# Optimization experiments

Hardware: AMD Instinct MI355X
Metric: run time of the kernel (lower is better)

Reference implementation:

```python
import jax, jax.numpy as jnp
import numpy as np

B, S, H, M, E = 8, 2048, 2048, 256, 8
Hh = H // 2

def setup_inputs() -> dict:
    key = jax.random.key(0)
    ks = jax.random.split(key, 12)
    s = 0.02
    return {
        "x":   jax.random.normal(ks[0], (B, S, H), dtype=jnp.float32),
        # metacognitive (router) network: H -> M -> M -> E, softmax
        "Wm1": jax.random.normal(ks[1], (H, M), dtype=jnp.float32) * s,
        "bm1": jnp.zeros((M,), dtype=jnp.float32),
        "Wm2": jax.random.normal(ks[2], (M, M), dtype=jnp.float32) * s,
        "bm2": jnp.zeros((M,), dtype=jnp.float32),
        "Wm3": jax.random.normal(ks[3], (M, E), dtype=jnp.float32) * s,
        "bm3": jnp.zeros((E,), dtype=jnp.float32),
        # stacked expert MLPs: Linear(H,H/2)-ReLU-Linear(H/2,H)-Tanh
        "W1":  jax.random.normal(ks[4], (E, H, Hh), dtype=jnp.float32) * s,
        "b1":  jnp.zeros((E, Hh), dtype=jnp.float32),
        "W2":  jax.random.normal(ks[5], (E, Hh, H), dtype=jnp.float32) * s,
        "b2":  jnp.zeros((E, H), dtype=jnp.float32),
        # strategy_effectiveness buffer (init: ones)
        "eff": jnp.ones((E,), dtype=jnp.float32),
    }

def reference(x, Wm1, bm1, Wm2, bm2, Wm3, bm3, W1, b1, W2, b2, eff):
    # --- select_strategy ---
    pooled = x.mean(axis=1)                                   # [B,H]
    h = jax.nn.relu(pooled @ Wm1 + bm1)                       # [B,M]
    h = jax.nn.relu(h @ Wm2 + bm2)                            # [B,M]
    probs = jax.nn.softmax(h @ Wm3 + bm3, axis=-1)            # [B,E]
    w = jax.nn.softmax(probs * eff[None, :], axis=-1)         # [B,E]
    # --- apply_strategies (all experts batched) ---
    he = jax.nn.relu(jnp.einsum('bsh,ehf->bsef', x, W1) + b1) # [B,S,E,Hh]
    ye = jnp.tanh(jnp.einsum('bsef,efh->bseh', he, W2) + b2)  # [B,S,E,H]
    out = jnp.einsum('bseh,be->bsh', ye, w)                   # [B,S,H]
    return out
```

## Files before the change

kernel.cpp:

```cpp
#include <hip/hip_runtime.h>
#include <hip/hip_bf16.h>
#include <cstdint>
#include <cstddef>

#define B_   8
#define S_   2048
#define H_   2048
#define M_   256
#define E_   8
#define HH_  1024
#define BS_  (B_*S_)

typedef _Float16 f16;
typedef _Float16 f16x8 __attribute__((ext_vector_type(8)));
typedef _Float16 f16x4 __attribute__((ext_vector_type(4)));
typedef float    f32x4 __attribute__((ext_vector_type(4)));

#define HSLOT 32768

__device__ __forceinline__ void gl_lds16(const void* g, void* l) {
  __builtin_amdgcn_global_load_lds(
      (const __attribute__((address_space(1))) uint32_t*)g,
      (__attribute__((address_space(3))) uint32_t*)l, 16, 0, 0);
}

__device__ __forceinline__ float fast_tanh(float x) {
  x = fminf(fmaxf(x, -15.f), 15.f);
  float t = __expf(2.f * x);
  return (t - 1.f) / (t + 1.f);
}

template<int NG, bool SEG, int KB, class F>
__device__ __forceinline__ void kloop(const char* aBlk, const char* bBlk,
                                      char* ldsc, f32x4 (&acc)[8][4], F&& fold) {
  constexpr int NH = NG * 2;
  const int tid = threadIdx.x, ln = tid & 63, wv = tid >> 6;
  const int l15 = ln & 15, kq = ln >> 4;
  const int wm = wv >> 2, wn = wv & 3;

  const char* aPc[2]; const char* bPc[2];
#pragma unroll
  for (int j = 0; j < 2; ++j) {
    int row = (tid >> 2) + j * 128;
    int kqs = (tid & 3) ^ ((row >> 1) & 3);
    aPc[j] = aBlk + (size_t)row * KB + kqs * 16;
    bPc[j] = bBlk + (size_t)row * KB + kqs * 16;
  }
  const int rowA = wm * 128 + l15;
  const int rowB = wn * 64 + l15;
  const int aRd = rowA * 64 + ((kq ^ ((rowA >> 1) & 3)) << 4);
  const int bRd = 16384 + rowB * 64 + ((kq ^ ((rowB >> 1) & 3)) << 4);
  const int dst0 = tid * 16;

  auto stage2 = [&](int Ht, int op) {
    if (Ht >= NH) return;
    char* sb = ldsc + (Ht & 3) * HSLOT;
    size_t oa, ob;
    if constexpr (SEG) {
      size_t kb = (size_t)((Ht & 31) * 64);
      oa = ((size_t)(Ht >> 5) << 25) + kb;
      ob = ((size_t)(Ht >> 5) << 22) + kb;
    } else { oa = ob = (size_t)Ht * 64; }
    if (op == 0) {
      gl_lds16(aPc[0] + oa, sb + dst0);
      gl_lds16(aPc[1] + oa, sb + 8192 + dst0);
    } else {
      gl_lds16(bPc[0] + ob, sb + 16384 + dst0);
      gl_lds16(bPc[1] + ob, sb + 24576 + dst0);
    }
  };

#pragma unroll
  for (int Ht = 0; Ht < 3; ++Ht) { stage2(Ht, 0); stage2(Ht, 1); }
  asm volatile("s_waitcnt vmcnt(8)" ::: "memory");
  __builtin_amdgcn_s_barrier();

#pragma unroll 1
  for (int g = 0; g < NG; ++g) {
#pragma unroll
    for (int kh = 0; kh < 2; ++kh) {
      const int H = g * 2 + kh;
      const char* sb = ldsc + (H & 3) * HSLOT;
      f16x8 bf[4];
#pragma unroll
      for (int mh = 0; mh < 2; ++mh) {
        f16x8 af[4];
        const char* ab = sb + aRd + mh * 4096;
#pragma unroll
        for (int m = 0; m < 4; ++m) af[m] = *(const f16x8*)(ab + m * 1024);
        if (mh == 0) {
          const char* bb = sb + bRd;
#pragma unroll
          for (int n = 0; n < 4; ++n) bf[n] = *(const f16x8*)(bb + n * 1024);
        }
        stage2(H + 3, mh);
        __builtin_amdgcn_s_barrier();
        __builtin_amdgcn_s_setprio(1);
#pragma unroll
        for (int m = 0; m < 4; ++m)
#pragma unroll
          for (int n = 0; n < 4; ++n)
            acc[mh * 4 + m][n] = __builtin_amdgcn_mfma_f32_16x16x32_f16(
                af[m], bf[n], acc[mh * 4 + m][n], 0, 0, 0);
        __builtin_amdgcn_s_setprio(0);
        if (mh == 1) {
          if (H < NH - 3)       { asm volatile("s_waitcnt vmcnt(8)" ::: "memory"); }
          else if (H == NH - 3) { asm volatile("s_waitcnt vmcnt(4)" ::: "memory"); }
          else if (H == NH - 2) { asm volatile("s_waitcnt vmcnt(0)" ::: "memory"); }
        }
        __builtin_amdgcn_s_barrier();
      }
    }
    if constexpr (SEG) { if ((g & 15) == 15) fold(g >> 4); }
  }
}

__global__ __launch_bounds__(512, 2) void gemm1_t8(
    const f16* __restrict__ xf, const f16* __restrict__ W1t,
    const float* __restrict__ b1, f16* __restrict__ he) {
  __shared__ alignas(16) char ldsc[4 * HSLOT];
  int id = blockIdx.x;
  int logical = (id & 7) * 256 + (id >> 3);
  int e = logical >> 8, mt = (logical >> 2) & 63, nt = logical & 3;
  int brow = mt * 256, bcol = nt * 256;

  const char* aBlk = (const char*)xf + (size_t)brow * 4096;
  const char* bBlk = (const char*)W1t + ((size_t)e << 22) + (size_t)bcol * 4096;

  f32x4 acc[8][4] = {};
  kloop<32, false, 4096>(aBlk, bBlk, ldsc, acc, [](int) {});

  const int tid = threadIdx.x, ln = tid & 63, wv = tid >> 6;
  const int l15 = ln & 15, kq4 = (ln >> 4) * 4;
  const int wm = wv >> 2, wn = wv & 3;
  f16* C = he + ((size_t)e << 24);
#pragma unroll
  for (int n = 0; n < 4; ++n) {
    int gc = bcol + wn * 64 + n * 16 + l15;
    float bias = b1[e * HH_ + gc];
#pragma unroll
    for (int m = 0; m < 8; ++m) {
      int gr0 = brow + wm * 128 + m * 16 + kq4;
#pragma unroll
      for (int r = 0; r < 4; ++r)
        C[(size_t)(gr0 + r) * HH_ + gc] = (f16)fmaxf(acc[m][n][r] + bias, 0.f);
    }
  }
}

__global__ __launch_bounds__(512, 2) void gemm2_t8(
    const f16* __restrict__ he, const f16* __restrict__ W2t,
    const float* __restrict__ b2, const float* __restrict__ wbuf,
    float* __restrict__ out) {
  __shared__ alignas(16) char ldsc[4 * HSLOT];
  __shared__ float biasLDS[E_][256];
  __shared__ float wLDS[E_];
  int id = blockIdx.x;
  int logical = (id & 7) * 64 + (id >> 3);
  int mt = logical >> 3, nt = logical & 7;
  int brow = mt * 256, bcol = nt * 256;
  int bb = brow >> 11;

  const int tid = threadIdx.x, ln = tid & 63, wv = tid >> 6;
  const int l15 = ln & 15, kq4 = (ln >> 4) * 4;
  const int wm = wv >> 2, wn = wv & 3;

  {
    int i = tid;
#pragma unroll
    for (int rep = 0; rep < 4; ++rep, i += 512)
      biasLDS[i >> 8][i & 255] = b2[(size_t)(i >> 8) * H_ + bcol + (i & 255)];
    if (tid < E_) wLDS[tid] = wbuf[bb * E_ + tid];
  }
  __syncthreads();

  const char* aBlk = (const char*)he + (size_t)brow * 2048;
  const char* bBlk = (const char*)W2t + (size_t)bcol * 2048;

  f32x4 acc[8][4] = {};
  f16x4 tot[8][4] = {};

  auto fold = [&](int e) {
    float we = wLDS[e];
#pragma unroll
    for (int n = 0; n < 4; ++n) {
      float bias = biasLDS[e][wn * 64 + n * 16 + l15];
#pragma unroll
      for (int m = 0; m < 8; ++m) {
#pragma unroll
        for (int r = 0; r < 4; ++r) {
          tot[m][n][r] += (f16)(we * fast_tanh(acc[m][n][r] + bias));
          acc[m][n][r] = 0.f;
        }
      }
    }
  };

  kloop<128, true, 2048>(aBlk, bBlk, ldsc, acc, fold);

#pragma unroll
  for (int n = 0; n < 4; ++n) {
    int gc = bcol + wn * 64 + n * 16 + l15;
#pragma unroll
    for (int m = 0; m < 8; ++m) {
      int gr0 = brow + wm * 128 + m * 16 + kq4;
#pragma unroll
      for (int r = 0; r < 4; ++r)
        out[(size_t)(gr0 + r) * H_ + gc] = (float)tot[m][n][r];
    }
  }
}

__global__ void convert_x_pool(const float* __restrict__ x, f16* __restrict__ xf,
                               float* __restrict__ partial) {
  int h  = blockIdx.x * 256 + threadIdx.x;
  int sc = blockIdx.y;
  int b  = blockIdx.z;
  size_t base = ((size_t)b * S_ + sc * 64) * H_ + h;
  float sum = 0.f;
#pragma unroll 4
  for (int i = 0; i < 64; ++i) {
    float v = x[base + (size_t)i * H_];
    sum += v;
    xf[base + (size_t)i * H_] = (f16)v;
  }
  partial[((size_t)b * H_ + h) * 32 + sc] = sum;
}

__global__ void pool_finalize(const float* __restrict__ partial, float* __restrict__ pooled) {
  int i = blockIdx.x * 256 + threadIdx.x;
  float s = 0.f;
#pragma unroll
  for (int c = 0; c < 32; ++c) s += partial[(size_t)i * 32 + c];
  pooled[i] = s * (1.0f / S_);
}

__global__ void router_kernel(const float* __restrict__ pooled,
                              const float* __restrict__ Wm1, const float* __restrict__ bm1,
                              const float* __restrict__ Wm2, const float* __restrict__ bm2,
                              const float* __restrict__ Wm3, const float* __restrict__ bm3,
                              const float* __restrict__ eff, float* __restrict__ wout) {
  __shared__ float pl[H_];
  __shared__ float h1[M_];
  __shared__ float h2[M_];
  __shared__ float lg[E_];
  int b = blockIdx.x;
  int t = threadIdx.x;

  for (int i = t; i < H_; i += 256) pl[i] = pooled[b * H_ + i];
  __syncthreads();

  float s = bm1[t];
  for (int k = 0; k < H_; ++k) s += pl[k] * Wm1[(size_t)k * M_ + t];
  h1[t] = fmaxf(s, 0.f);
  __syncthreads();

  s = bm2[t];
  for (int k = 0; k < M_; ++k) s += h1[k] * Wm2[k * M_ + t];
  h2[t] = fmaxf(s, 0.f);
  __syncthreads();

  if (t < E_) {
    float l = bm3[t];
    for (int k = 0; k < M_; ++k) l += h2[k] * Wm3[k * E_ + t];
    lg[t] = l;
  }
  __syncthreads();

  if (t == 0) {
    float p[E_], q[E_];
    float mx = -1e30f;
    for (int e = 0; e < E_; ++e) mx = fmaxf(mx, lg[e]);
    float den = 0.f;
    for (int e = 0; e < E_; ++e) { p[e] = __expf(lg[e] - mx); den += p[e]; }
    float inv = 1.f / den;
    for (int e = 0; e < E_; ++e) q[e] = p[e] * inv * eff[e];
    mx = -1e30f;
    for (int e = 0; e < E_; ++e) mx = fmaxf(mx, q[e]);
    den = 0.f;
    for (int e = 0; e < E_; ++e) { q[e] = __expf(q[e] - mx); den += q[e]; }
    inv = 1.f / den;
    for (int e = 0; e < E_; ++e) wout[b * E_ + e] = q[e] * inv;
  }
}

__global__ void transpose_cvt(const float* __restrict__ in, f16* __restrict__ out,
                              int R, int C) {
  __shared__ f16 tile[32][33];
  int e  = blockIdx.z;
  int c0 = blockIdx.x * 32, r0 = blockIdx.y * 32;
  int tx = threadIdx.x & 31, ty = threadIdx.x >> 5;
  const float* inp = in + (size_t)e * R * C;
  f16* outp = out + (size_t)e * R * C;
#pragma unroll
  for (int i = 0; i < 4; ++i) {
    int r = r0 + ty + i * 8;
    tile[ty + i * 8][tx] = (f16)inp[(size_t)r * C + c0 + tx];
  }
  __syncthreads();
#pragma unroll
  for (int i = 0; i < 4; ++i) {
    int c = c0 + ty + i * 8;
    outp[(size_t)c * R + r0 + tx] = tile[tx][ty + i * 8];
  }
}

extern "C" void kernel_launch(void* const* d_in, const int* in_sizes, int n_in,
                              void* d_out, int out_size, void* d_ws, size_t ws_size,
                              hipStream_t stream) {
  const float* x   = (const float*)d_in[0];
  const float* Wm1 = (const float*)d_in[1];
  const float* bm1 = (const float*)d_in[2];
  const float* Wm2 = (const float*)d_in[3];
  const float* bm2 = (const float*)d_in[4];
  const float* Wm3 = (const float*)d_in[5];
  const float* bm3 = (const float*)d_in[6];
  const float* W1  = (const float*)d_in[7];
  const float* b1  = (const float*)d_in[8];
  const float* W2  = (const float*)d_in[9];
  const float* b2  = (const float*)d_in[10];
  const float* eff = (const float*)d_in[11];
  float* out = (float*)d_out;

  char* ws = (char*)d_ws;
  size_t off = 0;
  auto take = [&](size_t bytes) { void* p = ws + off; off += (bytes + 255) & ~(size_t)255; return p; };

  f16*   xf      = (f16*)  take((size_t)BS_ * H_ * 2);
  f16*   W1t     = (f16*)  take((size_t)E_ * HH_ * H_ * 2);
  f16*   W2t     = (f16*)  take((size_t)E_ * H_ * HH_ * 2);
  float* partial = (float*)take((size_t)B_ * H_ * 32 * 4);
  float* pooled  = (float*)take((size_t)B_ * H_ * 4);
  float* wbuf    = (float*)take(1024);
  f16*   he      = (f16*)  take((size_t)E_ * BS_ * HH_ * 2);

  convert_x_pool<<<dim3(H_ / 256, S_ / 64, B_), 256, 0, stream>>>(x, xf, partial);
  pool_finalize<<<(B_ * H_) / 256, 256, 0, stream>>>(partial, pooled);
  router_kernel<<<B_, 256, 0, stream>>>(pooled, Wm1, bm1, Wm2, bm2, Wm3, bm3, eff, wbuf);
  transpose_cvt<<<dim3(HH_ / 32, H_ / 32, E_), 256, 0, stream>>>(W1, W1t, H_, HH_);
  transpose_cvt<<<dim3(H_ / 32, HH_ / 32, E_), 256, 0, stream>>>(W2, W2t, HH_, H_);

  gemm1_t8<<<2048, 512, 0, stream>>>(xf, W1t, b1, he);
  gemm2_t8<<<512, 512, 0, stream>>>(he, W2t, b2, wbuf, out);
}
```

Baseline: 1.420 ms.

## Double-buffer LDS fragment registers to overlap LDS reads with MFMA in k-loop

Restructures the GEMM k-loop so register fragments for the next half-tile are read from LDS while MFMAs run on the current fragments, using ping-pong register sets (af0/af1, bfE/bfO). It removes one of the two barriers per half-step and retunes the vmcnt waits to the new issue order of global-to-LDS loads. This costs more live registers, which may pressure occupancy at 2 waves/SIMD with 512 threads. The reduced barrier count also makes LDS slot reuse correctness depend on the new wait placement.

```diff
diff --git a/kernel.cpp b/kernel.cpp
--- a/kernel.cpp
+++ b/kernel.cpp
@@ -70,47 +70,83 @@
     }
   };
 
-#pragma unroll
-  for (int Ht = 0; Ht < 3; ++Ht) { stage2(Ht, 0); stage2(Ht, 1); }
+  f16x8 af0[4], af1[4], bfE[4], bfO[4];
+
+#pragma unroll
+  for (int t = 0; t < 3; ++t) { stage2(t, 0); stage2(t, 1); }
   asm volatile("s_waitcnt vmcnt(8)" ::: "memory");
   __builtin_amdgcn_s_barrier();
+  {
+    const char* s0 = ldsc;
+#pragma unroll
+    for (int m = 0; m < 4; ++m) af0[m] = *(const f16x8*)(s0 + aRd + m * 1024);
+#pragma unroll
+    for (int n = 0; n < 4; ++n) bfE[n] = *(const f16x8*)(s0 + bRd + n * 1024);
+  }
 
 #pragma unroll 1
   for (int g = 0; g < NG; ++g) {
-#pragma unroll
-    for (int kh = 0; kh < 2; ++kh) {
-      const int H = g * 2 + kh;
-      const char* sb = ldsc + (H & 3) * HSLOT;
-      f16x8 bf[4];
-#pragma unroll
-      for (int mh = 0; mh < 2; ++mh) {
-        f16x8 af[4];
-        const char* ab = sb + aRd + mh * 4096;
-#pragma unroll
-        for (int m = 0; m < 4; ++m) af[m] = *(const f16x8*)(ab + m * 1024);
-        if (mh == 0) {
-          const char* bb = sb + bRd;
-#pragma unroll
-          for (int n = 0; n < 4; ++n) bf[n] = *(const f16x8*)(bb + n * 1024);
-        }
-        stage2(H + 3, mh);
-        __builtin_amdgcn_s_barrier();
-        __builtin_amdgcn_s_setprio(1);
-#pragma unroll
-        for (int m = 0; m < 4; ++m)
-#pragma unroll
-          for (int n = 0; n < 4; ++n)
-            acc[mh * 4 + m][n] = __builtin_amdgcn_mfma_f32_16x16x32_f16(
-                af[m], bf[n], acc[mh * 4 + m][n], 0, 0, 0);
-        __builtin_amdgcn_s_setprio(0);
-        if (mh == 1) {
-          if (H < NH - 3)       { asm volatile("s_waitcnt vmcnt(8)" ::: "memory"); }
-          else if (H == NH - 3) { asm volatile("s_waitcnt vmcnt(4)" ::: "memory"); }
-          else if (H == NH - 2) { asm volatile("s_waitcnt vmcnt(0)" ::: "memory"); }
-        }
-        __builtin_amdgcn_s_barrier();
-      }
-    }
+    const int H0 = 2 * g;
+    const char* s0 = ldsc + (H0 & 3) * HSLOT;
+    const char* s1 = ldsc + ((H0 + 1) & 3) * HSLOT;
+
+#pragma unroll
+    for (int m = 0; m < 4; ++m) af1[m] = *(const f16x8*)(s0 + aRd + 4096 + m * 1024);
+    stage2(H0 + 3, 0);
+    __builtin_amdgcn_s_setprio(1);
+#pragma unroll
+    for (int m = 0; m < 4; ++m)
+#pragma unroll
+      for (int n = 0; n < 4; ++n)
+        acc[m][n] = __builtin_amdgcn_mfma_f32_16x16x32_f16(af0[m], bfE[n], acc[m][n], 0, 0, 0);
+    __builtin_amdgcn_s_setprio(0);
+
+    if (g < NG - 1) { asm volatile("s_waitcnt vmcnt(6)" ::: "memory"); }
+    else            { asm volatile("s_waitcnt vmcnt(0)" ::: "memory"); }
+    __builtin_amdgcn_s_barrier();
+#pragma unroll
+    for (int m = 0; m < 4; ++m) af0[m] = *(const f16x8*)(s1 + aRd + m * 1024);
+#pragma unroll
+    for (int n = 0; n < 4; ++n) bfO[n] = *(const f16x8*)(s1 + bRd + n * 1024);
+    stage2(H0 + 3, 1);
+    __builtin_amdgcn_s_setprio(1);
+#pragma unroll
+    for (int m = 0; m < 4; ++m)
+#pragma unroll
+      for (int n = 0; n < 4; ++n)
+        acc[4 + m][n] = __builtin_amdgcn_mfma_f32_16x16x32_f16(af1[m], bfE[n], acc[4 + m][n], 0, 0, 0);
+    __builtin_amdgcn_s_setprio(0);
+
+#pragma unroll
+    for (int m = 0; m < 4; ++m) af1[m] = *(const f16x8*)(s1 + aRd + 4096 + m * 1024);
+    stage2(H0 + 4, 0);
+    __builtin_amdgcn_s_setprio(1);
+#pragma unroll
+    for (int m = 0; m < 4; ++m)
+#pragma unroll
+      for (int n = 0; n < 4; ++n)
+        acc[m][n] = __builtin_amdgcn_mfma_f32_16x16x32_f16(af0[m], bfO[n], acc[m][n], 0, 0, 0);
+    __builtin_amdgcn_s_setprio(0);
+
+    if (g < NG - 1) {
+      if (g < NG - 2) { asm volatile("s_waitcnt vmcnt(6)" ::: "memory"); }
+      else            { asm volatile("s_waitcnt vmcnt(4)" ::: "memory"); }
+      __builtin_amdgcn_s_barrier();
+      const char* s2 = ldsc + ((H0 + 2) & 3) * HSLOT;
+#pragma unroll
+      for (int m = 0; m < 4; ++m) af0[m] = *(const f16x8*)(s2 + aRd + m * 1024);
+#pragma unroll
+      for (int n = 0; n < 4; ++n) bfE[n] = *(const f16x8*)(s2 + bRd + n * 1024);
+    }
+    stage2(H0 + 4, 1);
+    __builtin_amdgcn_s_setprio(1);
+#pragma unroll
+    for (int m = 0; m < 4; ++m)
+#pragma unroll
+      for (int n = 0; n < 4; ++n)
+        acc[4 + m][n] = __builtin_amdgcn_mfma_f32_16x16x32_f16(af1[m], bfO[n], acc[4 + m][n], 0, 0, 0);
+    __builtin_amdgcn_s_setprio(0);
+
     if constexpr (SEG) { if ((g & 15) == 15) fold(g >> 4); }
   }
 }
```

New measurement: 1.777 ms. 1.25x slower.
